# Kernel optimization log

Hardware: AMD Instinct MI355X
Metric: run time of the kernel (lower is better)

## Reference

```python
import jax, jax.numpy as jnp
import numpy as np

B, S, ENC = 64, 2048, 1024          # batch, encoder seq len, encoder feature dim
U, E_DIM, V_SZ = 512, 256, 50000    # dec_units, embedding_dim, vocab_size
IN_DIM = ENC + E_DIM                # LSTM input: [context ; token embedding]


def setup_inputs() -> dict:
    key = jax.random.key(0)
    ks = jax.random.split(key, 16)
    g = lambda k, shp, s=0.02: (jax.random.normal(k, shp, jnp.float32) * s)
    return {
        "x": jax.random.randint(ks[0], (B, 1), 0, V_SZ),
        "c_fwd": g(ks[1], (B, U), 0.1),
        "c_bwd": g(ks[2], (B, U), 0.1),
        "enc_output": jax.random.normal(ks[3], (B, S, ENC), jnp.float32),
        "emb": g(ks[4], (V_SZ, E_DIM)),
        "W1_w": g(ks[5], (ENC, U)), "W1_b": jnp.zeros((U,), jnp.float32),
        "W2_w": g(ks[6], (U, U)),   "W2_b": jnp.zeros((U,), jnp.float32),
        "W3_w": g(ks[7], (U, U)),   "W3_b": jnp.zeros((U,), jnp.float32),
        "V_w": g(ks[8], (U, 1)),    "V_b": jnp.zeros((1,), jnp.float32),
        "Kf": g(ks[9], (IN_DIM, 4 * U)),  "bf": jnp.zeros((4 * U,), jnp.float32),
        "Kb": g(ks[10], (IN_DIM, 4 * U)), "bb": jnp.zeros((4 * U,), jnp.float32),
        "fc_w": g(ks[11], (2 * U, V_SZ)), "fc_b": jnp.zeros((V_SZ,), jnp.float32),
    }


def _lstm_step_zero_state(xin, K, b):
    # Keras LSTM single step from zero (h0, c0): recurrent term vanishes.
    # Gate order in Keras kernel: i, f, c(g), o.
    z = xin @ K + b
    i, f, g, o = jnp.split(z, 4, axis=-1)
    i, o = jax.nn.sigmoid(i), jax.nn.sigmoid(o)  # f gate multiplies c0=0
    c = i * jnp.tanh(g)
    h = o * jnp.tanh(c)
    return h, c


def reference(x, c_fwd, c_bwd, enc_output, emb,
              W1_w, W1_b, W2_w, W2_b, W3_w, W3_b, V_w, V_b,
              Kf, bf, Kb, bb, fc_w, fc_b):
    # Bahdanau additive attention: score [B, S, 1]
    hidden_proj = (c_fwd @ W2_w + W2_b + c_bwd @ W3_w + W3_b)[:, None, :]  # [B,1,U]
    score = jnp.tanh(enc_output @ W1_w + W1_b + hidden_proj) @ V_w + V_b
    attn = jax.nn.softmax(score, axis=1)                 # softmax over S
    ctx = jnp.sum(attn * enc_output, axis=1)             # [B, ENC]

    xe = emb[x[:, 0]]                                    # [B, E_DIM]
    xin = jnp.concatenate([ctx, xe], axis=-1)            # [B, ENC+E_DIM]

    # Bidirectional LSTM over a length-1 sequence from zero initial state:
    # both directions see the same single timestep with separate weights.
    hf, cf = _lstm_step_zero_state(xin, Kf, bf)
    hb, cb = _lstm_step_zero_state(xin, Kb, bb)

    out = jnp.concatenate([hf, hb], axis=-1)             # [B, 2U]
    logits = out @ fc_w + fc_b                           # [B, vocab]
    return logits, hf, cf, hb, cb
```

## Files before the change

### kernel.cpp

```cpp
#include <hip/hip_runtime.h>

using u16 = unsigned short;
typedef float f32x4 __attribute__((ext_vector_type(4)));
typedef float f32x16 __attribute__((ext_vector_type(16)));
typedef __bf16 bf16x8 __attribute__((ext_vector_type(8)));
typedef u16 u16x8 __attribute__((ext_vector_type(8)));
typedef u16 u16x4 __attribute__((ext_vector_type(4)));

static constexpr int OF_HPB   = 262144;
static constexpr int OF_CTXP  = 294912;
static constexpr int OF_STATS = 2392064;
static constexpr int OF_XIN   = 2394112;
static constexpr int OF_ZPART = 2476032;
static constexpr int OF_HHL   = 3000320;
static constexpr size_t SCRATCH_FLOATS = 3065856;
static constexpr size_t SCRATCH_BYTES  = SCRATCH_FLOATS * 4ull;

__device__ __forceinline__ u16 f2bf(float f) {
  unsigned u = __float_as_uint(f);
  u += 0x7FFFu + ((u >> 16) & 1u);
  return (u16)(u >> 16);
}
__device__ __forceinline__ float bf2f(u16 u) {
  return __uint_as_float((unsigned)u << 16);
}
__device__ __forceinline__ float fast_tanh(float x) {
  x = fminf(fmaxf(x, -20.f), 20.f);
  float e = __expf(2.f * x);
  return (e - 1.f) / (e + 1.f);
}
__device__ __forceinline__ float fast_sig(float x) { return 1.f / (1.f + __expf(-x)); }

__global__ void k_prep(const float* __restrict__ W1w, u16* __restrict__ w1p,
                       const float* __restrict__ cf, const float* __restrict__ cb,
                       const float* __restrict__ W2w, const float* __restrict__ W2b,
                       const float* __restrict__ W3w, const float* __restrict__ W3b,
                       const float* __restrict__ W1b, float* __restrict__ hpb) {
  __shared__ float tile[16][516];
  const int t = threadIdx.x;
  if (blockIdx.x < 64) {
    const int ks = blockIdx.x;
    {
      int kk = t >> 4, u0 = (t & 15) * 32;
      const float* src = W1w + (size_t)(ks * 16 + kk) * 512 + u0;
      #pragma unroll
      for (int i = 0; i < 8; ++i)
        *(float4*)&tile[kk][u0 + i * 4] = *(const float4*)(src + i * 4);
    }
    __syncthreads();
    #pragma unroll
    for (int q = 0; q < 4; ++q) {
      int c = t + q * 256;
      int ug = c >> 6, l = c & 63;
      int u = ug * 32 + (l & 31), koct = l >> 5;
      u16x8 p;
      #pragma unroll
      for (int e = 0; e < 8; ++e) p[e] = f2bf(tile[koct * 8 + e][u]);
      *(u16x8*)(w1p + (size_t)ks * 8192 + (size_t)c * 8) = p;
    }
  } else {
    float* cfl = &tile[0][0];
    float* cbl = &tile[0][0] + 512;
    const int b = blockIdx.x - 64;
    cfl[t] = cf[(size_t)b * 512 + t];       cfl[t + 256] = cf[(size_t)b * 512 + t + 256];
    cbl[t] = cb[(size_t)b * 512 + t];       cbl[t + 256] = cb[(size_t)b * 512 + t + 256];
    __syncthreads();
    const int u1 = t, u2 = t + 256;
    float a1 = W2b[u1] + W3b[u1] + W1b[u1];
    float a2 = W2b[u2] + W3b[u2] + W1b[u2];
    for (int k = 0; k < 512; ++k) {
      float c1 = cfl[k], c2 = cbl[k];
      const float* r2 = W2w + (size_t)k * 512;
      const float* r3 = W3w + (size_t)k * 512;
      a1 += c1 * r2[u1] + c2 * r3[u1];
      a2 += c1 * r2[u2] + c2 * r3[u2];
    }
    hpb[(size_t)b * 512 + u1] = a1;
    hpb[(size_t)b * 512 + u2] = a2;
  }
}

__global__ void __launch_bounds__(1024, 8)
k_attn(const float* __restrict__ enc, const u16* __restrict__ w1p,
       const float* __restrict__ hpb, const float* __restrict__ Vw,
       const float* __restrict__ Vb, float* __restrict__ ctxp,
       float* __restrict__ stats) {
  __shared__ __align__(16) u16 smem[8448];

  const int t = threadIdx.x;
  const int bid = blockIdx.x;
  const int b = bid >> 5, tile = bid & 31;
  const size_t row0 = (size_t)b * 2048 + (size_t)tile * 64;

  const int l = t & 63, wv = t >> 6;

  const u16* bbase = w1p + (size_t)wv * 512 + (size_t)l * 8;

  const int sr = t >> 4, sq4 = t & 15;
  const float* a_src = enc + (row0 + sr) * 1024 + sq4 * 4;
  const int sm = sq4 >> 2, skoct = (sq4 >> 1) & 1, ssq = sq4 & 1;
  const int a_dst = sm * 1032 + (sr >> 5) * 512 + ((sr & 31) + skoct * 32) * 8 + ssq * 4;

  f32x16 acc0, acc1;
  #pragma unroll
  for (int i = 0; i < 16; ++i) { acc0[i] = 0.f; acc1[i] = 0.f; }

  float4 pv0, pv1;
  bf16x8 bcur[4], bnxt[4];
  {
    float4 v = *(const float4*)(a_src);
    u16x4 w4;
    w4[0] = f2bf(v.x); w4[1] = f2bf(v.y); w4[2] = f2bf(v.z); w4[3] = f2bf(v.w);
    *(u16x4*)(smem + a_dst) = w4;
    pv0 = *(const float4*)(a_src + 64);
    pv1 = *(const float4*)(a_src + 128);
    #pragma unroll
    for (int m = 0; m < 4; ++m)
      bcur[m] = *(const bf16x8*)(bbase + (size_t)m * 8192);
  }
  asm volatile("s_waitcnt lgkmcnt(0)" ::: "memory");
  __builtin_amdgcn_s_barrier();
  __builtin_amdgcn_sched_barrier(0);

  for (int km = 0; km < 16; ++km) {
    const int cur = km & 1;
    if (km < 15) {
      u16x4 w4;
      w4[0] = f2bf(pv0.x); w4[1] = f2bf(pv0.y); w4[2] = f2bf(pv0.z); w4[3] = f2bf(pv0.w);
      *(u16x4*)(smem + (cur ^ 1) * 4128 + a_dst) = w4;
      pv0 = pv1;
      if (km < 13) pv1 = *(const float4*)(a_src + (km + 3) * 64);
      #pragma unroll
      for (int m = 0; m < 4; ++m)
        bnxt[m] = *(const bf16x8*)(bbase + (size_t)((km + 1) * 4 + m) * 8192);
    }
    const u16* Ac = smem + cur * 4128;
    #pragma unroll
    for (int m = 0; m < 4; ++m) {
      bf16x8 a0 = *(const bf16x8*)(Ac + m * 1032 + l * 8);
      bf16x8 a1 = *(const bf16x8*)(Ac + m * 1032 + 512 + l * 8);
      acc0 = __builtin_amdgcn_mfma_f32_32x32x16_bf16(a0, bcur[m], acc0, 0, 0, 0);
      acc1 = __builtin_amdgcn_mfma_f32_32x32x16_bf16(a1, bcur[m], acc1, 0, 0, 0);
    }
    #pragma unroll
    for (int m = 0; m < 4; ++m) bcur[m] = bnxt[m];
    asm volatile("s_waitcnt lgkmcnt(0)" ::: "memory");
    __builtin_amdgcn_s_barrier();
    __builtin_amdgcn_sched_barrier(0);
  }

  float* fsm = (float*)smem;
  float* red = fsm;
  float* scv = fsm + 1088;
  float* pcv = fsm + 1152;

  const int ucol = (wv << 5) + (l & 31);
  const float vwv = Vw[ucol];
  const float hpv = hpb[(size_t)b * 512 + ucol];
  const int hi4 = (l >> 5) * 4;
  const bool writer = ((l & 31) == 0);
  #pragma unroll
  for (int im = 0; im < 2; ++im) {
    #pragma unroll
    for (int r = 0; r < 16; ++r) {
      float s = vwv * fast_tanh((im ? acc1[r] : acc0[r]) + hpv);
      s += __shfl_xor(s, 1);
      s += __shfl_xor(s, 2);
      s += __shfl_xor(s, 4);
      s += __shfl_xor(s, 8);
      s += __shfl_xor(s, 16);
      if (writer) {
        int sl = im * 32 + (r & 3) + 8 * (r >> 2) + hi4;
        red[sl * 17 + wv] = s;
      }
    }
  }
  __syncthreads();
  if (t < 64) {
    float s = Vb[0];
    #pragma unroll
    for (int wq = 0; wq < 16; ++wq) s += red[t * 17 + wq];
    float e = __expf(s);
    scv[t] = e;
    float p = e;
    p += __shfl_xor(p, 1);  p += __shfl_xor(p, 2);  p += __shfl_xor(p, 4);
    p += __shfl_xor(p, 8);  p += __shfl_xor(p, 16); p += __shfl_xor(p, 32);
    if (t == 0) stats[bid] = p;
  }
  __syncthreads();

  {
    const int c4 = (t & 255) * 4;
    const int rq = t >> 8;
    const float* ep = enc + (row0 + rq * 16) * 1024 + c4;
    float ax = 0.f, ay = 0.f, az = 0.f, aw2 = 0.f;
    #pragma unroll 4
    for (int r = 0; r < 16; ++r) {
      float4 v = *(const float4*)(ep + (size_t)r * 1024);
      float sc = scv[rq * 16 + r];
      ax += sc * v.x; ay += sc * v.y; az += sc * v.z; aw2 += sc * v.w;
    }
    if (rq) {
      float4 st = {ax, ay, az, aw2};
      *(float4*)&pcv[(rq - 1) * 1024 + c4] = st;
    }
    __syncthreads();
    if (rq == 0) {
      float4 p1 = *(const float4*)&pcv[c4];
      float4 p2 = *(const float4*)&pcv[1024 + c4];
      float4 p3 = *(const float4*)&pcv[2048 + c4];
      float4 o = {ax + p1.x + p2.x + p3.x, ay + p1.y + p2.y + p3.y,
                  az + p1.z + p2.z + p3.z, aw2 + p1.w + p2.w + p3.w};
      *(float4*)&ctxp[(size_t)bid * 1024 + c4] = o;
    }
  }
}

__global__ void k_attn_reduce(const float* __restrict__ ctxp, const float* __restrict__ stats,
                              const int* __restrict__ x, const float* __restrict__ emb,
                              float* __restrict__ xin) {
  __shared__ float ps[32];
  __shared__ float invs;
  const int b = blockIdx.x, t = threadIdx.x;
  if (t < 32) ps[t] = stats[b * 32 + t];
  __syncthreads();
  if (t == 0) {
    float s = 0.f;
    #pragma unroll
    for (int i = 0; i < 32; ++i) s += ps[i];
    invs = 1.f / s;
  }
  __syncthreads();
  const float inv = invs;
  #pragma unroll
  for (int i = 0; i < 4; ++i) {
    int c = t + i * 256;
    float a = 0.f;
    for (int chv = 0; chv < 32; ++chv)
      a += ctxp[((size_t)b * 32 + chv) * 1024 + c];
    xin[(size_t)b * 1280 + c] = a * inv;
  }
  xin[(size_t)b * 1280 + 1024 + t] = emb[(size_t)x[b] * 256 + t];
}

__global__ void k_lstm_gemm(const float* __restrict__ xin, const float* __restrict__ Kf,
                            const float* __restrict__ Kb, float* __restrict__ zpart) {
  __shared__ float xl[32][68];
  const int t = threadIdx.x;
  const int bid = blockIdx.x;
  const int dir = bid >> 7;
  const int jt  = (bid >> 1) & 63;
  const int ks  = bid & 1;
  const float* K = dir ? Kb : Kf;
  const int j  = jt * 32 + (t & 31);
  const int tb = t >> 5;
  const int brow = t >> 2, kq = (t & 3) * 8;
  float acc[8] = {0,0,0,0,0,0,0,0};
  for (int k0 = ks * 640; k0 < ks * 640 + 640; k0 += 32) {
    float4 x0 = *(const float4*)&xin[(size_t)brow * 1280 + k0 + kq];
    float4 x1 = *(const float4*)&xin[(size_t)brow * 1280 + k0 + kq + 4];
    __syncthreads();
    xl[kq+0][brow]=x0.x; xl[kq+1][brow]=x0.y; xl[kq+2][brow]=x0.z; xl[kq+3][brow]=x0.w;
    xl[kq+4][brow]=x1.x; xl[kq+5][brow]=x1.y; xl[kq+6][brow]=x1.z; xl[kq+7][brow]=x1.w;
    __syncthreads();
    const float* Kp = K + (size_t)k0 * 2048 + j;
    #pragma unroll 8
    for (int kk = 0; kk < 32; ++kk) {
      float wv = Kp[(size_t)kk * 2048];
      float4 v0 = *(const float4*)&xl[kk][tb * 8];
      float4 v1 = *(const float4*)&xl[kk][tb * 8 + 4];
      acc[0] += v0.x * wv; acc[1] += v0.y * wv; acc[2] += v0.z * wv; acc[3] += v0.w * wv;
      acc[4] += v1.x * wv; acc[5] += v1.y * wv; acc[6] += v1.z * wv; acc[7] += v1.w * wv;
    }
  }
  float* zp = zpart + ((size_t)dir * 2 + ks) * 64 * 2048;
  #pragma unroll
  for (int i = 0; i < 8; ++i)
    zp[(size_t)(tb * 8 + i) * 2048 + j] = acc[i];
}

__global__ void k_gates(const float* __restrict__ zpart, const float* __restrict__ bfv,
                        const float* __restrict__ bbv, float* __restrict__ dout,
                        u16* __restrict__ hhl) {
  const int dir = blockIdx.x >> 6, b = blockIdx.x & 63, u = threadIdx.x;
  const float* bias = dir ? bbv : bfv;
  const float* z0 = zpart + ((size_t)dir * 2 + 0) * 131072 + (size_t)b * 2048;
  const float* z1 = zpart + ((size_t)dir * 2 + 1) * 131072 + (size_t)b * 2048;
  float zi = z0[u]        + z1[u]        + bias[u];
  float zg = z0[1024 + u] + z1[1024 + u] + bias[1024 + u];
  float zo = z0[1536 + u] + z1[1536 + u] + bias[1536 + u];
  float c = fast_sig(zi) * fast_tanh(zg);
  float h = fast_sig(zo) * fast_tanh(c);
  size_t base = 3200000u + (size_t)dir * 65536u;
  dout[base + (size_t)b * 512 + u] = h;
  dout[base + 32768u + (size_t)b * 512 + u] = c;
  u16 hi = f2bf(h);
  u16 lo = f2bf(h - bf2f(hi));
  hhl[(size_t)b * 1024 + dir * 512 + u] = hi;
  hhl[65536u + (size_t)b * 1024 + dir * 512 + u] = lo;
}

__global__ void __launch_bounds__(256)
k_fc_mfma(const float* __restrict__ fcw, const u16* __restrict__ hhl,
          const float* __restrict__ fcb, float* __restrict__ logits) {
  __shared__ float Bs[2][32 * 136];
  const int t = threadIdx.x;
  const int j0 = blockIdx.x * 128;
  const int l = t & 63, w = t >> 6;
  const int ln = l & 15, lg = l >> 4;
  const int srow = t >> 3, scol = (t & 7) * 16;
  const bool interior = (j0 + 128 <= 50000);

  f32x4 acc[4][2];
  #pragma unroll
  for (int im = 0; im < 4; ++im)
    #pragma unroll
    for (int nf = 0; nf < 2; ++nf) acc[im][nf] = f32x4{0.f, 0.f, 0.f, 0.f};

  float4 pre[4];
  {
    const float* src = fcw + (size_t)srow * 50000 + j0 + scol;
    if (interior) {
      #pragma unroll
      for (int q = 0; q < 4; ++q) pre[q] = *(const float4*)(src + q * 4);
    } else {
      #pragma unroll
      for (int q = 0; q < 4; ++q) {
        int jb = j0 + scol + q * 4;
        pre[q].x = (jb + 0 < 50000) ? src[q*4 + 0] : 0.f;
        pre[q].y = (jb + 1 < 50000) ? src[q*4 + 1] : 0.f;
        pre[q].z = (jb + 2 < 50000) ? src[q*4 + 2] : 0.f;
        pre[q].w = (jb + 3 < 50000) ? src[q*4 + 3] : 0.f;
      }
    }
    #pragma unroll
    for (int q = 0; q < 4; ++q)
      *(float4*)&Bs[0][srow * 136 + scol + q * 4] = pre[q];
  }
  __syncthreads();

  for (int ks = 0; ks < 32; ++ks) {
    const int cur = ks & 1;
    if (ks < 31) {
      const float* src = fcw + (size_t)(ks + 1) * 32 * 50000 + (size_t)srow * 50000 + j0 + scol;
      if (interior) {
        #pragma unroll
        for (int q = 0; q < 4; ++q) pre[q] = *(const float4*)(src + q * 4);
      } else {
        #pragma unroll
        for (int q = 0; q < 4; ++q) {
          int jb = j0 + scol + q * 4;
          pre[q].x = (jb + 0 < 50000) ? src[q*4 + 0] : 0.f;
          pre[q].y = (jb + 1 < 50000) ? src[q*4 + 1] : 0.f;
          pre[q].z = (jb + 2 < 50000) ? src[q*4 + 2] : 0.f;
          pre[q].w = (jb + 3 < 50000) ? src[q*4 + 3] : 0.f;
        }
      }
    }
    bf16x8 ahi[4], alo[4];
    #pragma unroll
    for (int im = 0; im < 4; ++im) {
      const u16* ha = hhl + (size_t)(im * 16 + ln) * 1024 + ks * 32 + lg * 8;
      ahi[im] = *(const bf16x8*)(ha);
      alo[im] = *(const bf16x8*)(ha + 65536);
    }
    bf16x8 bfr[2];
    #pragma unroll
    for (int nf = 0; nf < 2; ++nf) {
      u16x8 pv;
      #pragma unroll
      for (int i = 0; i < 8; ++i)
        pv[i] = f2bf(Bs[cur][(lg * 8 + i) * 136 + w * 32 + nf * 16 + ln]);
      bfr[nf] = *(bf16x8*)&pv;
    }
    #pragma unroll
    for (int im = 0; im < 4; ++im)
      #pragma unroll
      for (int nf = 0; nf < 2; ++nf) {
        acc[im][nf] = __builtin_amdgcn_mfma_f32_16x16x32_bf16(alo[im], bfr[nf], acc[im][nf], 0, 0, 0);
        acc[im][nf] = __builtin_amdgcn_mfma_f32_16x16x32_bf16(ahi[im], bfr[nf], acc[im][nf], 0, 0, 0);
      }
    if (ks < 31) {
      #pragma unroll
      for (int q = 0; q < 4; ++q)
        *(float4*)&Bs[cur ^ 1][srow * 136 + scol + q * 4] = pre[q];
    }
    __syncthreads();
  }

  #pragma unroll
  for (int nf = 0; nf < 2; ++nf) {
    int c = j0 + w * 32 + nf * 16 + ln;
    if (c < 50000) {
      float fb = fcb[c];
      #pragma unroll
      for (int im = 0; im < 4; ++im)
        #pragma unroll
        for (int r = 0; r < 4; ++r) {
          int row = im * 16 + lg * 4 + r;
          logits[(size_t)row * 50000 + c] = acc[im][nf][r] + fb;
        }
    }
  }
}

__global__ void __launch_bounds__(256)
k_fc_f32(const float* __restrict__ dout_ro, const float* __restrict__ fcw,
         const float* __restrict__ fcb, float* __restrict__ logits) {
  __shared__ float ol[64][68];
  __shared__ float wl[64][132];
  const int t = threadIdx.x;
  const int j0 = blockIdx.x * 128;
  const int tb = t >> 5, tj = t & 31;
  const float* hf = dout_ro + 3200000u;
  const float* hb = dout_ro + 3200000u + 65536u;
  float acc[8][4];
  #pragma unroll
  for (int bi = 0; bi < 8; ++bi)
    #pragma unroll
    for (int ji = 0; ji < 4; ++ji) acc[bi][ji] = 0.f;

  for (int k0 = 0; k0 < 1024; k0 += 64) {
    __syncthreads();
    {
      int bb = t >> 2, kq = (t & 3) * 16;
      const float* src = (k0 < 512) ? (hf + (size_t)bb * 512 + k0 + kq)
                                    : (hb + (size_t)bb * 512 + (k0 - 512) + kq);
      #pragma unroll
      for (int i = 0; i < 4; ++i) {
        float4 v = *(const float4*)(src + i * 4);
        ol[kq + i*4 + 0][bb] = v.x;
        ol[kq + i*4 + 1][bb] = v.y;
        ol[kq + i*4 + 2][bb] = v.z;
        ol[kq + i*4 + 3][bb] = v.w;
      }
    }
    {
      int kk = t >> 2, jh = (t & 3) * 32;
      const float* wsrc = fcw + (size_t)(k0 + kk) * 50000 + j0 + jh;
      #pragma unroll
      for (int i = 0; i < 8; ++i) {
        int j = j0 + jh + i * 4;
        float4 v;
        if (j + 3 < 50000) {
          v = *(const float4*)(wsrc + i * 4);
        } else {
          v.x = (j + 0 < 50000) ? wsrc[i*4 + 0] : 0.f;
          v.y = (j + 1 < 50000) ? wsrc[i*4 + 1] : 0.f;
          v.z = (j + 2 < 50000) ? wsrc[i*4 + 2] : 0.f;
          v.w = 0.f;
        }
        *(float4*)&wl[kk][jh + i * 4] = v;
      }
    }
    __syncthreads();
    #pragma unroll 4
    for (int kk = 0; kk < 64; ++kk) {
      float4 wv = *(const float4*)&wl[kk][tj * 4];
      float4 q0 = *(const float4*)&ol[kk][tb * 8];
      float4 q1 = *(const float4*)&ol[kk][tb * 8 + 4];
      float obv[8] = {q0.x, q0.y, q0.z, q0.w, q1.x, q1.y, q1.z, q1.w};
      #pragma unroll
      for (int bi = 0; bi < 8; ++bi) {
        acc[bi][0] += obv[bi] * wv.x;
        acc[bi][1] += obv[bi] * wv.y;
        acc[bi][2] += obv[bi] * wv.z;
        acc[bi][3] += obv[bi] * wv.w;
      }
    }
  }

  const int j = j0 + tj * 4;
  if (j + 3 < 50000) {
    float4 fb = *(const float4*)(fcb + j);
    #pragma unroll
    for (int bi = 0; bi < 8; ++bi) {
      float4 r;
      r.x = acc[bi][0] + fb.x; r.y = acc[bi][1] + fb.y;
      r.z = acc[bi][2] + fb.z; r.w = acc[bi][3] + fb.w;
      *(float4*)&logits[(size_t)(tb * 8 + bi) * 50000 + j] = r;
    }
  } else {
    for (int ji = 0; ji < 4; ++ji) {
      if (j + ji < 50000) {
        float fb = fcb[j + ji];
        for (int bi = 0; bi < 8; ++bi)
          logits[(size_t)(tb * 8 + bi) * 50000 + j + ji] = acc[bi][ji] + fb;
      }
    }
  }
}

extern "C" void kernel_launch(void* const* d_in, const int* in_sizes, int n_in,
                              void* d_out, int out_size, void* d_ws, size_t ws_size,
                              hipStream_t stream) {
  const int*   x    = (const int*)  d_in[0];
  const float* cfwd = (const float*)d_in[1];
  const float* cbwd = (const float*)d_in[2];
  const float* enc  = (const float*)d_in[3];
  const float* emb  = (const float*)d_in[4];
  const float* W1w  = (const float*)d_in[5];
  const float* W1b  = (const float*)d_in[6];
  const float* W2w  = (const float*)d_in[7];
  const float* W2b  = (const float*)d_in[8];
  const float* W3w  = (const float*)d_in[9];
  const float* W3b  = (const float*)d_in[10];
  const float* Vw   = (const float*)d_in[11];
  const float* Vb   = (const float*)d_in[12];
  const float* Kf   = (const float*)d_in[13];
  const float* bfv  = (const float*)d_in[14];
  const float* Kb   = (const float*)d_in[15];
  const float* bbv  = (const float*)d_in[16];
  const float* fcw  = (const float*)d_in[17];
  const float* fcb  = (const float*)d_in[18];
  float* out = (float*)d_out;

  const bool haveWs = (ws_size >= SCRATCH_BYTES);
  float* S = haveWs ? (float*)d_ws : out;
  u16*   w1p   = (u16*)S;
  float* hpb   = S + OF_HPB;
  float* ctxp  = S + OF_CTXP;
  float* stats = S + OF_STATS;
  float* xin   = S + OF_XIN;
  float* zpart = S + OF_ZPART;
  u16*   hhl   = (u16*)(S + OF_HHL);

  k_prep<<<128, 256, 0, stream>>>(W1w, w1p, cfwd, cbwd, W2w, W2b, W3w, W3b, W1b, hpb);
  k_attn<<<2048, 1024, 0, stream>>>(enc, w1p, hpb, Vw, Vb, ctxp, stats);
  k_attn_reduce<<<64, 256, 0, stream>>>(ctxp, stats, x, emb, xin);
  k_lstm_gemm<<<256, 256, 0, stream>>>(xin, Kf, Kb, zpart);
  k_gates<<<128, 512, 0, stream>>>(zpart, bfv, bbv, out, hhl);
  if (haveWs) k_fc_mfma<<<392, 256, 0, stream>>>(fcw, hhl, fcb, out);
  else        k_fc_f32<<<391, 256, 0, stream>>>(out, fcw, fcb, out);
}
```

Baseline: 587.4 us.

## Halve attention block to 512 threads with 2x2 MFMA tiles per wave

The attention kernel now runs 8 waves per block instead of 16. Each wave computes a 64x64 output tile as a 2x2 grid of 32x32 MFMAs, so each A fragment read from shared memory is reused across two B fragments. Each thread now stages 8 floats of the encoder tile. The W1 B-operand register prefetch (bcur/bnxt) is removed and B is loaded directly from global inside the loop, which cuts register pressure but may expose load latency. The attention epilogue is reworked to match the new wave-to-column mapping and to use 8-wide loads.

```diff
diff --git a/kernel.cpp b/kernel.cpp
--- a/kernel.cpp
+++ b/kernel.cpp
@@ -80,7 +80,7 @@
   }
 }
 
-__global__ void __launch_bounds__(1024, 8)
+__global__ void __launch_bounds__(512, 4)
 k_attn(const float* __restrict__ enc, const u16* __restrict__ w1p,
        const float* __restrict__ hpb, const float* __restrict__ Vw,
        const float* __restrict__ Vb, float* __restrict__ ctxp,
@@ -94,29 +94,27 @@
 
   const int l = t & 63, wv = t >> 6;
 
-  const u16* bbase = w1p + (size_t)wv * 512 + (size_t)l * 8;
-
-  const int sr = t >> 4, sq4 = t & 15;
-  const float* a_src = enc + (row0 + sr) * 1024 + sq4 * 4;
-  const int sm = sq4 >> 2, skoct = (sq4 >> 1) & 1, ssq = sq4 & 1;
-  const int a_dst = sm * 1032 + (sr >> 5) * 512 + ((sr & 31) + skoct * 32) * 8 + ssq * 4;
-
-  f32x16 acc0, acc1;
+  const u16* bbase = w1p + (size_t)(wv * 2) * 512 + (size_t)l * 8;
+
+  const int sr = t >> 3, sq8 = t & 7;
+  const int sksl = sq8 >> 1, skoct = sq8 & 1;
+  const float* a_src = enc + (row0 + sr) * 1024 + sq8 * 8;
+  const int a_dst = sksl * 1032 + (sr >> 5) * 512 + ((sr & 31) + skoct * 32) * 8;
+
+  f32x16 acc00, acc01, acc10, acc11;
   #pragma unroll
-  for (int i = 0; i < 16; ++i) { acc0[i] = 0.f; acc1[i] = 0.f; }
-
-  float4 pv0, pv1;
-  bf16x8 bcur[4], bnxt[4];
+  for (int i = 0; i < 16; ++i) { acc00[i]=0.f; acc01[i]=0.f; acc10[i]=0.f; acc11[i]=0.f; }
+
+  float4 p00, p01;
   {
-    float4 v = *(const float4*)(a_src);
-    u16x4 w4;
-    w4[0] = f2bf(v.x); w4[1] = f2bf(v.y); w4[2] = f2bf(v.z); w4[3] = f2bf(v.w);
-    *(u16x4*)(smem + a_dst) = w4;
-    pv0 = *(const float4*)(a_src + 64);
-    pv1 = *(const float4*)(a_src + 128);
-    #pragma unroll
-    for (int m = 0; m < 4; ++m)
-      bcur[m] = *(const bf16x8*)(bbase + (size_t)m * 8192);
+    float4 v0 = *(const float4*)(a_src);
+    float4 v1 = *(const float4*)(a_src + 4);
+    u16x8 pk;
+    pk[0]=f2bf(v0.x); pk[1]=f2bf(v0.y); pk[2]=f2bf(v0.z); pk[3]=f2bf(v0.w);
+    pk[4]=f2bf(v1.x); pk[5]=f2bf(v1.y); pk[6]=f2bf(v1.z); pk[7]=f2bf(v1.w);
+    *(u16x8*)(smem + a_dst) = pk;
+    p00 = *(const float4*)(a_src + 64);
+    p01 = *(const float4*)(a_src + 68);
   }
   asm volatile("s_waitcnt lgkmcnt(0)" ::: "memory");
   __builtin_amdgcn_s_barrier();
@@ -125,25 +123,29 @@
   for (int km = 0; km < 16; ++km) {
     const int cur = km & 1;
     if (km < 15) {
-      u16x4 w4;
-      w4[0] = f2bf(pv0.x); w4[1] = f2bf(pv0.y); w4[2] = f2bf(pv0.z); w4[3] = f2bf(pv0.w);
-      *(u16x4*)(smem + (cur ^ 1) * 4128 + a_dst) = w4;
-      pv0 = pv1;
-      if (km < 13) pv1 = *(const float4*)(a_src + (km + 3) * 64);
-      #pragma unroll
-      for (int m = 0; m < 4; ++m)
-        bnxt[m] = *(const bf16x8*)(bbase + (size_t)((km + 1) * 4 + m) * 8192);
+      u16x8 pk;
+      pk[0]=f2bf(p00.x); pk[1]=f2bf(p00.y); pk[2]=f2bf(p00.z); pk[3]=f2bf(p00.w);
+      pk[4]=f2bf(p01.x); pk[5]=f2bf(p01.y); pk[6]=f2bf(p01.z); pk[7]=f2bf(p01.w);
+      *(u16x8*)(smem + (cur ^ 1) * 4128 + a_dst) = pk;
+      if (km < 14) {
+        const float* sp = a_src + (km + 2) * 64;
+        p00 = *(const float4*)(sp);
+        p01 = *(const float4*)(sp + 4);
+      }
     }
     const u16* Ac = smem + cur * 4128;
     #pragma unroll
     for (int m = 0; m < 4; ++m) {
       bf16x8 a0 = *(const bf16x8*)(Ac + m * 1032 + l * 8);
       bf16x8 a1 = *(const bf16x8*)(Ac + m * 1032 + 512 + l * 8);
-      acc0 = __builtin_amdgcn_mfma_f32_32x32x16_bf16(a0, bcur[m], acc0, 0, 0, 0);
-      acc1 = __builtin_amdgcn_mfma_f32_32x32x16_bf16(a1, bcur[m], acc1, 0, 0, 0);
-    }
-    #pragma unroll
-    for (int m = 0; m < 4; ++m) bcur[m] = bnxt[m];
+      const u16* bp = bbase + (size_t)(km * 4 + m) * 8192;
+      bf16x8 b0 = *(const bf16x8*)(bp);
+      bf16x8 b1 = *(const bf16x8*)(bp + 512);
+      acc00 = __builtin_amdgcn_mfma_f32_32x32x16_bf16(a0, b0, acc00, 0, 0, 0);
+      acc01 = __builtin_amdgcn_mfma_f32_32x32x16_bf16(a0, b1, acc01, 0, 0, 0);
+      acc10 = __builtin_amdgcn_mfma_f32_32x32x16_bf16(a1, b0, acc10, 0, 0, 0);
+      acc11 = __builtin_amdgcn_mfma_f32_32x32x16_bf16(a1, b1, acc11, 0, 0, 0);
+    }
     asm volatile("s_waitcnt lgkmcnt(0)" ::: "memory");
     __builtin_amdgcn_s_barrier();
     __builtin_amdgcn_sched_barrier(0);
@@ -151,27 +153,32 @@
 
   float* fsm = (float*)smem;
   float* red = fsm;
-  float* scv = fsm + 1088;
-  float* pcv = fsm + 1152;
-
-  const int ucol = (wv << 5) + (l & 31);
-  const float vwv = Vw[ucol];
-  const float hpv = hpb[(size_t)b * 512 + ucol];
-  const int hi4 = (l >> 5) * 4;
-  const bool writer = ((l & 31) == 0);
-  #pragma unroll
-  for (int im = 0; im < 2; ++im) {
-    #pragma unroll
-    for (int r = 0; r < 16; ++r) {
-      float s = vwv * fast_tanh((im ? acc1[r] : acc0[r]) + hpv);
-      s += __shfl_xor(s, 1);
-      s += __shfl_xor(s, 2);
-      s += __shfl_xor(s, 4);
-      s += __shfl_xor(s, 8);
-      s += __shfl_xor(s, 16);
-      if (writer) {
-        int sl = im * 32 + (r & 3) + 8 * (r >> 2) + hi4;
-        red[sl * 17 + wv] = s;
+  float* scv = fsm + 576;
+  float* pcv = fsm + 640;
+
+  {
+    const int lu = l & 31;
+    const float vw0 = Vw[wv * 64 + lu];
+    const float vw1 = Vw[wv * 64 + 32 + lu];
+    const float hp0 = hpb[(size_t)b * 512 + wv * 64 + lu];
+    const float hp1 = hpb[(size_t)b * 512 + wv * 64 + 32 + lu];
+    const int hi4 = (l >> 5) * 4;
+    const bool writer = (lu == 0);
+    #pragma unroll
+    for (int mi = 0; mi < 2; ++mi) {
+      #pragma unroll
+      for (int r = 0; r < 16; ++r) {
+        float s = vw0 * fast_tanh((mi ? acc10[r] : acc00[r]) + hp0)
+                + vw1 * fast_tanh((mi ? acc11[r] : acc01[r]) + hp1);
+        s += __shfl_xor(s, 1);
+        s += __shfl_xor(s, 2);
+        s += __shfl_xor(s, 4);
+        s += __shfl_xor(s, 8);
+        s += __shfl_xor(s, 16);
+        if (writer) {
+          int row = mi * 32 + (r & 3) + 8 * (r >> 2) + hi4;
+          red[row * 9 + wv] = s;
+        }
       }
     }
   }
@@ -179,7 +186,7 @@
   if (t < 64) {
     float s = Vb[0];
     #pragma unroll
-    for (int wq = 0; wq < 16; ++wq) s += red[t * 17 + wq];
+    for (int wq = 0; wq < 8; ++wq) s += red[t * 9 + wq];
     float e = __expf(s);
     scv[t] = e;
     float p = e;
@@ -190,28 +197,37 @@
   __syncthreads();
 
   {
-    const int c4 = (t & 255) * 4;
-    const int rq = t >> 8;
-    const float* ep = enc + (row0 + rq * 16) * 1024 + c4;
-    float ax = 0.f, ay = 0.f, az = 0.f, aw2 = 0.f;
+    const int c8 = (t & 127) * 8;
+    const int rq = t >> 7;
+    const float* ep = enc + (row0 + rq * 16) * 1024 + c8;
+    float a8[8] = {0.f,0.f,0.f,0.f,0.f,0.f,0.f,0.f};
     #pragma unroll 4
     for (int r = 0; r < 16; ++r) {
-      float4 v = *(const float4*)(ep + (size_t)r * 1024);
+      float4 v0 = *(const float4*)(ep + (size_t)r * 1024);
+      float4 v1 = *(const float4*)(ep + (size_t)r * 1024 + 4);
       float sc = scv[rq * 16 + r];
-      ax += sc * v.x; ay += sc * v.y; az += sc * v.z; aw2 += sc * v.w;
+      a8[0] += sc * v0.x; a8[1] += sc * v0.y; a8[2] += sc * v0.z; a8[3] += sc * v0.w;
+      a8[4] += sc * v1.x; a8[5] += sc * v1.y; a8[6] += sc * v1.z; a8[7] += sc * v1.w;
     }
     if (rq) {
-      float4 st = {ax, ay, az, aw2};
-      *(float4*)&pcv[(rq - 1) * 1024 + c4] = st;
+      float4 s0 = {a8[0], a8[1], a8[2], a8[3]};
+      float4 s1 = {a8[4], a8[5], a8[6], a8[7]};
+      *(float4*)&pcv[(rq - 1) * 1024 + c8] = s0;
+      *(float4*)&pcv[(rq - 1) * 1024 + c8 + 4] = s1;
     }
     __syncthreads();
     if (rq == 0) {
-      float4 p1 = *(const float4*)&pcv[c4];
-      float4 p2 = *(const float4*)&pcv[1024 + c4];
-      float4 p3 = *(const float4*)&pcv[2048 + c4];
-      float4 o = {ax + p1.x + p2.x + p3.x, ay + p1.y + p2.y + p3.y,
-                  az + p1.z + p2.z + p3.z, aw2 + p1.w + p2.w + p3.w};
-      *(float4*)&ctxp[(size_t)bid * 1024 + c4] = o;
+      float4 o0, o1;
+      o0.x = a8[0] + pcv[c8+0] + pcv[1024+c8+0] + pcv[2048+c8+0];
+      o0.y = a8[1] + pcv[c8+1] + pcv[1024+c8+1] + pcv[2048+c8+1];
+      o0.z = a8[2] + pcv[c8+2] + pcv[1024+c8+2] + pcv[2048+c8+2];
+      o0.w = a8[3] + pcv[c8+3] + pcv[1024+c8+3] + pcv[2048+c8+3];
+      o1.x = a8[4] + pcv[c8+4] + pcv[1024+c8+4] + pcv[2048+c8+4];
+      o1.y = a8[5] + pcv[c8+5] + pcv[1024+c8+5] + pcv[2048+c8+5];
+      o1.z = a8[6] + pcv[c8+6] + pcv[1024+c8+6] + pcv[2048+c8+6];
+      o1.w = a8[7] + pcv[c8+7] + pcv[1024+c8+7] + pcv[2048+c8+7];
+      *(float4*)&ctxp[(size_t)bid * 1024 + c8] = o0;
+      *(float4*)&ctxp[(size_t)bid * 1024 + c8 + 4] = o1;
     }
   }
 }
@@ -526,7 +542,7 @@
   u16*   hhl   = (u16*)(S + OF_HHL);
 
   k_prep<<<128, 256, 0, stream>>>(W1w, w1p, cfwd, cbwd, W2w, W2b, W3w, W3b, W1b, hpb);
-  k_attn<<<2048, 1024, 0, stream>>>(enc, w1p, hpb, Vw, Vb, ctxp, stats);
+  k_attn<<<2048, 512, 0, stream>>>(enc, w1p, hpb, Vw, Vb, ctxp, stats);
   k_attn_reduce<<<64, 256, 0, stream>>>(ctxp, stats, x, emb, xin);
   k_lstm_gemm<<<256, 256, 0, stream>>>(xin, Kf, Kb, zpart);
   k_gates<<<128, 512, 0, stream>>>(zpart, bfv, bbv, out, hhl);
```

Result: faster. 508.5 us (-13.4%).
